# Optimization experiments

Measured on AMD Instinct MI355X. Metric: run time of the kernel, lower is better.

The kernel has to match this reference:

```python
import jax, jax.numpy as jnp
import numpy as np

EPS = 1e-6
INV_T = 1.0
STEPS = 4
S = 1  # MD_S
R = 1  # MD_R


def setup_inputs() -> dict:
    key = jax.random.key(0)
    k1, k2 = jax.random.split(key)
    # NMF operates on non-negative data -> uniform [0,1)
    x = jax.random.uniform(k1, (4, 16, 160, 72, 72), dtype=jnp.float32)
    bases = jax.random.uniform(k2, (4 * S, 160 // S, R), dtype=jnp.float32)
    # _build_bases: F.normalize(bases, dim=1) -> L2 normalize over D axis
    bases = bases / jnp.maximum(jnp.linalg.norm(bases, axis=1, keepdims=True), 1e-12)
    return {"x": x, "bases": bases}


def _local_step(xr, bases, coef):
    # xr: [B, D, N], bases: [B, D, R], coef: [B, N, R]
    # multiplicative NMF update for coef
    num_c = jnp.einsum('bdn,bdr->bnr', xr, bases)                     # x^T b
    btb = jnp.einsum('bdr,bds->brs', bases, bases)                    # b^T b  [B,R,R]
    coef = coef * num_c / (jnp.einsum('bnr,brs->bns', coef, btb) + EPS)
    # multiplicative NMF update for bases
    num_b = jnp.einsum('bdn,bnr->bdr', xr, coef)                      # x c
    ctc = jnp.einsum('bnr,bns->brs', coef, coef)                      # c^T c  [B,R,R]
    bases = bases * num_b / (jnp.einsum('bdr,brs->bds', bases, ctc) + EPS)
    return bases, coef


def _compute_coef(xr, bases, coef):
    num_c = jnp.einsum('bdn,bdr->bnr', xr, bases)
    btb = jnp.einsum('bdr,bds->brs', bases, bases)
    return coef * num_c / (jnp.einsum('bnr,brs->bns', coef, btb) + EPS)


def reference(x, bases):
    B, C, T, H, W = x.shape
    D = T // S
    N = C * H * W
    xr = x.reshape(B * S, D, N)  # [4, 160, 82944]

    def local_inference(xr, bases):
        coef = jax.nn.softmax(INV_T * jnp.einsum('bdn,bdr->bnr', xr, bases), axis=-1)
        for _ in range(STEPS):
            bases, coef = _local_step(xr, bases, coef)
        return bases, coef

    # local_inference is @torch.no_grad() in the original
    bases_f, coef = jax.lax.stop_gradient(local_inference(xr, bases))
    coef = _compute_coef(xr, bases_f, coef)
    out = jnp.einsum('bdr,bnr->bdn', bases_f, coef)  # bases @ coef^T
    return out.reshape(B, C, T, H, W)
```

## Files before the change

### kernel.cpp

```cpp
#include <hip/hip_runtime.h>
#include <hip/hip_bf16.h>

#define EPS 1e-6f

constexpr int D  = 160;
constexpr int NN = 82944;
constexpr int B  = 4;

typedef __bf16 bf16x8 __attribute__((ext_vector_type(8)));
typedef __bf16 bf16x4 __attribute__((ext_vector_type(4)));
typedef float  floatx4 __attribute__((ext_vector_type(4)));

constexpr int BK = 64;
constexpr int BKP = BK + 8;
constexpr int SLABS = 8;
constexpr int COLS_PER_BLOCK = BK * SLABS;
constexpr int GRAM_BLOCKS = NN / COLS_PER_BLOCK;

__global__ __launch_bounds__(256, 2)
void gram_kernel(const float* __restrict__ x, float* __restrict__ P)
{
    __shared__ __align__(16) __bf16 xs[D * BKP];

    const int tid = threadIdx.x;
    const int batch = blockIdx.y;
    const int w  = tid >> 6;
    const int l  = tid & 63;
    const int lr = l & 15;
    const int lq = l >> 4;
    const int itile0 = (w & 1) * 5;
    const int jtile0 = (w >> 1) * 5;
    const int srow = tid >> 4;
    const int scol = (tid & 15) * 4;

    const float* xb = x + (size_t)batch * D * NN + (size_t)blockIdx.x * COLS_PER_BLOCK;
    const float* pbase = xb + (size_t)srow * NN + scol;

    floatx4 acc[5][5] = {};
    float4 pf[10];

    #pragma unroll
    for (int p = 0; p < 10; ++p)
        pf[p] = *(const float4*)(pbase + (size_t)p * 16 * NN);

    for (int s = 0; s < SLABS; ++s) {
        __syncthreads();
        #pragma unroll
        for (int p = 0; p < 10; ++p) {
            bf16x4 h = { (__bf16)pf[p].x, (__bf16)pf[p].y, (__bf16)pf[p].z, (__bf16)pf[p].w };
            *(bf16x4*)&xs[(srow + p * 16) * BKP + scol] = h;
        }
        __syncthreads();
        if (s + 1 < SLABS) {
            const float* pn = pbase + (s + 1) * BK;
            #pragma unroll
            for (int p = 0; p < 10; ++p)
                pf[p] = *(const float4*)(pn + (size_t)p * 16 * NN);
        }
        #pragma unroll
        for (int k = 0; k < BK / 32; ++k) {
            bf16x8 fa[5], fb[5];
            #pragma unroll
            for (int i = 0; i < 5; ++i) {
                fa[i] = *(const bf16x8*)&xs[((itile0 + i) * 16 + lr) * BKP + k * 32 + lq * 8];
                fb[i] = *(const bf16x8*)&xs[((jtile0 + i) * 16 + lr) * BKP + k * 32 + lq * 8];
            }
            #pragma unroll
            for (int i = 0; i < 5; ++i)
                #pragma unroll
                for (int j = 0; j < 5; ++j)
                    acc[i][j] = __builtin_amdgcn_mfma_f32_16x16x32_bf16(fa[i], fb[j], acc[i][j], 0, 0, 0);
        }
    }

    float* Pb = P + ((size_t)batch * GRAM_BLOCKS + blockIdx.x) * (size_t)(D * D);
    #pragma unroll
    for (int i = 0; i < 5; ++i) {
        const int d1base = (itile0 + i) * 16 + lq * 4;
        #pragma unroll
        for (int j = 0; j < 5; ++j) {
            const int d2 = (jtile0 + j) * 16 + lr;
            #pragma unroll
            for (int r = 0; r < 4; ++r)
                __builtin_nontemporal_store(acc[i][j][r], &Pb[(size_t)(d1base + r) * D + d2]);
        }
    }
}

__global__ __launch_bounds__(256)
void reduce_kernel(const float* __restrict__ P, float* __restrict__ G)
{
    const int batch = blockIdx.y;
    const int i4 = (blockIdx.x * 256 + threadIdx.x) * 4;
    const float* p = P + (size_t)batch * GRAM_BLOCKS * D * D + i4;
    floatx4 s = {0.f, 0.f, 0.f, 0.f};
    #pragma unroll 9
    for (int k = 0; k < GRAM_BLOCKS; ++k)
        s += __builtin_nontemporal_load((const floatx4*)(p + (size_t)k * D * D));
    *(floatx4*)(G + (size_t)batch * D * D + i4) = s;
}

__device__ __forceinline__ float block_reduce_bcast(float v, float* red)
{
    #pragma unroll
    for (int off = 32; off > 0; off >>= 1)
        v += __shfl_xor(v, off, 64);
    const int w = threadIdx.x >> 6;
    if ((threadIdx.x & 63) == 0) red[w] = v;
    __syncthreads();
    float s = red[0] + red[1] + red[2] + red[3];
    __syncthreads();
    return s;
}

__global__ __launch_bounds__(256)
void iter_kernel(const float* __restrict__ bases, const float* __restrict__ G,
                 float* __restrict__ bvec, float* __restrict__ svec)
{
    __shared__ float bs[D];
    __shared__ float red[4];
    const int batch = blockIdx.x;
    const int tid = threadIdx.x;
    const float* Gb = G + (size_t)batch * D * D;

    if (tid < D) bs[tid] = bases[batch * D + tid];
    __syncthreads();

    for (int step = 0; step < 4; ++step) {
        float v = (tid < D) ? bs[tid] * bs[tid] : 0.0f;
        const float btb = block_reduce_bcast(v, red);
        const float gamma = btb + EPS;

        float m = 0.0f;
        if (tid < D) {
            const float* row = Gb + (size_t)tid * D;
            #pragma unroll 8
            for (int j = 0; j < D; j += 4) {
                float4 g4 = *(const float4*)(row + j);
                m += g4.x * bs[j] + g4.y * bs[j + 1] + g4.z * bs[j + 2] + g4.w * bs[j + 3];
            }
        }
        float bm = (tid < D) ? bs[tid] * m : 0.0f;
        const float beta = block_reduce_bcast(bm, red);
        const float ctc = beta / (gamma * gamma);

        __syncthreads();
        if (tid < D) {
            const float bd = bs[tid];
            bs[tid] = bd * (m / gamma) / (bd * ctc + EPS);
        }
        __syncthreads();
    }

    float v = (tid < D) ? bs[tid] * bs[tid] : 0.0f;
    const float btb = block_reduce_bcast(v, red);
    const float inv = 1.0f / (btb + EPS);
    if (tid < D) {
        bvec[batch * D + tid] = bs[tid];
        svec[batch * D + tid] = bs[tid] * inv;
    }
}

__global__ __launch_bounds__(256)
void out_kernel(const float* __restrict__ x, const float* __restrict__ bvec,
                const float* __restrict__ svec, float* __restrict__ out)
{
    __shared__ float bsh[D], ssh[D];
    __shared__ floatx4 partA[256];
    __shared__ floatx4 partB[256];

    const int tid = threadIdx.x;
    const int batch = blockIdx.y;
    const int g = tid >> 5;
    const int lane = tid & 31;
    const size_t base0 = (size_t)batch * D * NN + (size_t)blockIdx.x * 256 + lane * 4;
    const size_t base1 = base0 + 128;

    if (tid < D) { bsh[tid] = bvec[batch * D + tid]; ssh[tid] = svec[batch * D + tid]; }
    __syncthreads();

    floatx4 t0 = {0.f, 0.f, 0.f, 0.f};
    floatx4 t1 = {0.f, 0.f, 0.f, 0.f};
    #pragma unroll
    for (int d = g; d < D; d += 8) {
        floatx4 xv0 = *(const floatx4*)(x + base0 + (size_t)d * NN);
        floatx4 xv1 = *(const floatx4*)(x + base1 + (size_t)d * NN);
        const float bd = bsh[d];
        t0 += xv0 * bd;
        t1 += xv1 * bd;
    }
    partA[tid] = t0;
    partB[tid] = t1;
    __syncthreads();
    if (tid < 32) {
        floatx4 s = partA[tid];
        #pragma unroll
        for (int k = 1; k < 8; ++k) s += partA[k * 32 + tid];
        partA[tid] = s;
    } else if (tid < 64) {
        floatx4 s = partB[tid - 32];
        #pragma unroll
        for (int k = 1; k < 8; ++k) s += partB[k * 32 + (tid - 32)];
        partB[tid - 32] = s;
    }
    __syncthreads();
    t0 = partA[lane];
    t1 = partB[lane];

    #pragma unroll
    for (int d = g; d < D; d += 8) {
        const float sd = ssh[d];
        floatx4 o0 = t0 * sd;
        floatx4 o1 = t1 * sd;
        __builtin_nontemporal_store(o0, (floatx4*)(out + base0 + (size_t)d * NN));
        __builtin_nontemporal_store(o1, (floatx4*)(out + base1 + (size_t)d * NN));
    }
}

extern "C" void kernel_launch(void* const* d_in, const int* in_sizes, int n_in,
                              void* d_out, int out_size, void* d_ws, size_t ws_size,
                              hipStream_t stream)
{
    (void)in_sizes; (void)n_in; (void)out_size; (void)ws_size;
    const float* x     = (const float*)d_in[0];
    const float* bases = (const float*)d_in[1];
    float* out = (float*)d_out;

    float* P    = (float*)d_out;
    float* G    = (float*)d_out + (size_t)50000000;
    float* bvec = (float*)d_ws;
    float* svec = bvec + B * D;

    gram_kernel<<<dim3(GRAM_BLOCKS, B), 256, 0, stream>>>(x, P);
    reduce_kernel<<<dim3(25, B), 256, 0, stream>>>(P, G);
    iter_kernel<<<dim3(B), 256, 0, stream>>>(bases, G, bvec, svec);
    out_kernel<<<dim3(NN / 256, B), 256, 0, stream>>>(x, bvec, svec, out);
}
```

Measured before the change: 446.8 us.

## Double-buffer gram LDS tiles and store partials in fragment order

The gram kernel now alternates between two LDS buffers, which removes one of the two barriers per slab so that writes of the next slab can overlap reads of the current one. Partial Gram tiles are written as contiguous float4 fragments in MFMA accumulator order instead of scattered scalar stores. The reduce kernel un-permutes the fragment layout when it writes G. The cost is doubled LDS use, which may limit occupancy at two blocks per CU, and a scattered scalar write pattern in the small reduce kernel.

```diff
diff --git a/kernel.cpp b/kernel.cpp
--- a/kernel.cpp
+++ b/kernel.cpp
@@ -20,7 +20,7 @@
 __global__ __launch_bounds__(256, 2)
 void gram_kernel(const float* __restrict__ x, float* __restrict__ P)
 {
-    __shared__ __align__(16) __bf16 xs[D * BKP];
+    __shared__ __align__(16) __bf16 xs[2][D * BKP];
 
     const int tid = threadIdx.x;
     const int batch = blockIdx.y;
@@ -44,26 +44,26 @@
         pf[p] = *(const float4*)(pbase + (size_t)p * 16 * NN);
 
     for (int s = 0; s < SLABS; ++s) {
-        __syncthreads();
+        __bf16* buf = xs[s & 1];
         #pragma unroll
         for (int p = 0; p < 10; ++p) {
             bf16x4 h = { (__bf16)pf[p].x, (__bf16)pf[p].y, (__bf16)pf[p].z, (__bf16)pf[p].w };
-            *(bf16x4*)&xs[(srow + p * 16) * BKP + scol] = h;
-        }
-        __syncthreads();
+            *(bf16x4*)&buf[(srow + p * 16) * BKP + scol] = h;
+        }
         if (s + 1 < SLABS) {
             const float* pn = pbase + (s + 1) * BK;
             #pragma unroll
             for (int p = 0; p < 10; ++p)
                 pf[p] = *(const float4*)(pn + (size_t)p * 16 * NN);
         }
+        __syncthreads();
         #pragma unroll
         for (int k = 0; k < BK / 32; ++k) {
             bf16x8 fa[5], fb[5];
             #pragma unroll
             for (int i = 0; i < 5; ++i) {
-                fa[i] = *(const bf16x8*)&xs[((itile0 + i) * 16 + lr) * BKP + k * 32 + lq * 8];
-                fb[i] = *(const bf16x8*)&xs[((jtile0 + i) * 16 + lr) * BKP + k * 32 + lq * 8];
+                fa[i] = *(const bf16x8*)&buf[((itile0 + i) * 16 + lr) * BKP + k * 32 + lq * 8];
+                fb[i] = *(const bf16x8*)&buf[((jtile0 + i) * 16 + lr) * BKP + k * 32 + lq * 8];
             }
             #pragma unroll
             for (int i = 0; i < 5; ++i)
@@ -73,31 +73,39 @@
         }
     }
 
-    float* Pb = P + ((size_t)batch * GRAM_BLOCKS + blockIdx.x) * (size_t)(D * D);
-    #pragma unroll
-    for (int i = 0; i < 5; ++i) {
-        const int d1base = (itile0 + i) * 16 + lq * 4;
-        #pragma unroll
-        for (int j = 0; j < 5; ++j) {
-            const int d2 = (jtile0 + j) * 16 + lr;
-            #pragma unroll
-            for (int r = 0; r < 4; ++r)
-                __builtin_nontemporal_store(acc[i][j][r], &Pb[(size_t)(d1base + r) * D + d2]);
-        }
-    }
+    float* Pb = P + ((size_t)batch * GRAM_BLOCKS + blockIdx.x) * (size_t)(D * D)
+                  + w * 6400 + l * 4;
+    #pragma unroll
+    for (int i = 0; i < 5; ++i)
+        #pragma unroll
+        for (int j = 0; j < 5; ++j)
+            __builtin_nontemporal_store(acc[i][j], (floatx4*)(Pb + (i * 5 + j) * 256));
 }
 
 __global__ __launch_bounds__(256)
 void reduce_kernel(const float* __restrict__ P, float* __restrict__ G)
 {
     const int batch = blockIdx.y;
-    const int i4 = (blockIdx.x * 256 + threadIdx.x) * 4;
-    const float* p = P + (size_t)batch * GRAM_BLOCKS * D * D + i4;
+    const int f4 = (blockIdx.x * 256 + threadIdx.x) * 4;
+    const float* p = P + (size_t)batch * GRAM_BLOCKS * D * D + f4;
     floatx4 s = {0.f, 0.f, 0.f, 0.f};
     #pragma unroll 9
     for (int k = 0; k < GRAM_BLOCKS; ++k)
         s += __builtin_nontemporal_load((const floatx4*)(p + (size_t)k * D * D));
-    *(floatx4*)(G + (size_t)batch * D * D + i4) = s;
+
+    const int w   = f4 / 6400;
+    const int rem = f4 % 6400;
+    const int t   = rem / 256;
+    const int q   = rem % 256;
+    const int i   = t / 5;
+    const int j   = t % 5;
+    const int l   = q >> 2;
+    const int d1b = (w & 1) * 80 + i * 16 + (l >> 4) * 4;
+    const int d2  = (w >> 1) * 80 + j * 16 + (l & 15);
+    float* Gb = G + (size_t)batch * D * D;
+    #pragma unroll
+    for (int r = 0; r < 4; ++r)
+        Gb[(size_t)(d1b + r) * D + d2] = s[r];
 }
 
 __device__ __forceinline__ float block_reduce_bcast(float v, float* red)
```

Result: no change. 440.3 us (-1.5%).
